# Kernel tuning notes

Hardware: AMD Instinct MI355X
Metric: run time of the kernel (lower is better)

The kernel has to match this reference:

```python
import jax, jax.numpy as jnp
import numpy as np

NEG = -1e30

def setup_inputs() -> dict:
    key = jax.random.key(0)
    ks = jax.random.split(key, 6)
    B, H, Lc, Lq = 32, 256, 1024, 256
    C = jax.random.normal(ks[0], (B, H, Lc), dtype=jnp.float32)
    Q = jax.random.normal(ks[1], (B, H, Lq), dtype=jnp.float32)
    cmask = jnp.ones((B, Lc), dtype=jnp.int32)
    qmask = jnp.ones((B, Lq), dtype=jnp.int32)
    # xavier_uniform on [3H,1]: bound = sqrt(6/(3H+1))
    bound = float(np.sqrt(6.0 / (3 * H + 1)))
    w = jax.random.uniform(ks[2], (3 * H,), minval=-bound, maxval=bound, dtype=jnp.float32)
    # kaiming_normal (relu, fan_in=4H): std = sqrt(2/(4H))
    W_res = jax.random.normal(ks[3], (H, 4 * H), dtype=jnp.float32) * float(np.sqrt(2.0 / (4 * H)))
    b_res = jnp.zeros((H,), dtype=jnp.float32)
    return {"C": C, "Q": Q, "cmask": cmask, "qmask": qmask, "w": w, "W_res": W_res, "b_res": b_res}

def reference(C, Q, cmask, qmask, w, W_res, b_res):
    H = w.shape[0] // 3
    Ct = jnp.transpose(C, (0, 2, 1))  # [B, Lc, H]
    Qt = jnp.transpose(Q, (0, 2, 1))  # [B, Lq, H]
    w1, w2, w3 = w[:H], w[H:2 * H], w[2 * H:]
    # trilinear similarity S[b,i,j] = Ct_i.w1 + Qt_j.w2 + (Ct_i*Qt_j).w3
    S = (jnp.einsum('blh,h->bl', Ct, w1)[:, :, None]
         + jnp.einsum('bmh,h->bm', Qt, w2)[:, None, :]
         + jnp.einsum('blh,bmh->blm', Ct * w3, Qt))  # [B, Lc, Lq]
    qm = qmask.astype(jnp.float32)[:, None, :]  # [B,1,Lq]
    cm = cmask.astype(jnp.float32)[:, :, None]  # [B,Lc,1]
    S_row = jax.nn.softmax(S + NEG * (1.0 - qm), axis=2)   # over questions
    S_col = jax.nn.softmax(S + NEG * (1.0 - cm), axis=1)   # over context
    A = jnp.einsum('blm,bmh->blh', S_row, Qt)  # [B, Lc, H]
    Bm = jnp.einsum('blm,bkm->blk', S_row, S_col)  # [B, Lc, Lc]
    Bv = jnp.einsum('blk,bkh->blh', Bm, Ct)  # [B, Lc, H]
    cat = jnp.concatenate([Ct, A, Ct * A, Ct * Bv], axis=2)  # [B, Lc, 4H]
    out = jax.nn.relu(jnp.einsum('blf,hf->blh', cat, W_res) + b_res)
    return jnp.transpose(out, (0, 2, 1))  # [B, H, Lc]
```

## Files before the change

### kernel.cpp

```cpp
#include <hip/hip_runtime.h>
#include <math.h>

#define NB 32
#define NH 256
#define NLC 1024
#define NLQ 256
#define NEGV (-1e30f)
#define TCH 8
#define KSPLIT 4

typedef short short8 __attribute__((ext_vector_type(8)));
typedef float f32x4 __attribute__((ext_vector_type(4)));

__device__ inline short bf16_of(float f) {
  union { float f; unsigned u; } v;
  v.f = f;
  unsigned r = (v.u + 0x7fffu + ((v.u >> 16) & 1u)) >> 16;
  return (short)r;
}
__device__ inline float f_of(short s) {
  union { unsigned u; float f; } v;
  v.u = ((unsigned)(unsigned short)s) << 16;
  return v.f;
}
__device__ inline short8 cvt8(float4 a, float4 b) {
  short8 o;
  o[0] = bf16_of(a.x); o[1] = bf16_of(a.y); o[2] = bf16_of(a.z); o[3] = bf16_of(a.w);
  o[4] = bf16_of(b.x); o[5] = bf16_of(b.y); o[6] = bf16_of(b.z); o[7] = bf16_of(b.w);
  return o;
}

#define XCD_SWZ(GX, GY, GZ, bx, by, bz)                                 \
  int bx, by, bz;                                                       \
  {                                                                     \
    int _lin = blockIdx.x + (GX) * (blockIdx.y + (GY) * blockIdx.z);    \
    const int _nwg = (GX) * (GY) * (GZ);                                \
    _lin = (_lin & 7) * (_nwg >> 3) + (_lin >> 3);                      \
    bx = _lin % (GX);                                                   \
    by = (_lin / (GX)) % (GY);                                          \
    bz = _lin / ((GX) * (GY));                                          \
  }

__device__ inline void lds_w8(short* lds, int r, int c, short8 v) {
  int byteoff = (r << 6) + (((c ^ ((r >> 1) & 3)) & 3) << 4);
  *(short8*)((char*)lds + byteoff) = v;
}
__device__ inline short8 lds_r8(const short* lds, int R, int g) {
  int byteoff = (R << 6) + (((g ^ ((R >> 1) & 3)) & 3) << 4);
  return *(const short8*)((const char*)lds + byteoff);
}
__device__ inline void stage_g(const short* src, int ld, short* lds, int t) {
  int L = t & 63, w = t >> 6;
  int cp = (L & 3) ^ ((L >> 3) & 3);
#pragma unroll
  for (int i = 0; i < 2; ++i) {
    int seg = w + i * 4;
    const short* g = src + (size_t)(seg * 16 + (L >> 2)) * ld + cp * 8;
    __builtin_amdgcn_global_load_lds(
        (const __attribute__((address_space(1))) unsigned int*)g,
        (__attribute__((address_space(3))) unsigned int*)(lds + seg * 512), 16,
        0, 0);
  }
}

#define GEMM_IDS                                       \
  int t = threadIdx.x, lane = t & 63, w = t >> 6;      \
  int ln = lane & 15, g = lane >> 4;                   \
  int wr = (w >> 1) << 6, wc = (w & 1) << 6;           \
  (void)wr; (void)wc;

#define MFMA_STEP(AS, BS)                                                      \
  {                                                                            \
    short8 af[4], bfr[4];                                                      \
    _Pragma("unroll") for (int mi = 0; mi < 4; ++mi) af[mi] =                  \
        lds_r8(AS, wr + mi * 16 + ln, g);                                      \
    _Pragma("unroll") for (int ni = 0; ni < 4; ++ni) bfr[ni] =                 \
        lds_r8(BS, wc + ni * 16 + ln, g);                                      \
    _Pragma("unroll") for (int mi = 0; mi < 4; ++mi)                           \
        _Pragma("unroll") for (int ni = 0; ni < 4; ++ni) acc[mi][ni] =         \
            __builtin_amdgcn_mfma_f32_16x16x32_bf16(af[mi], bfr[ni],           \
                                                    acc[mi][ni], 0, 0, 0);     \
  }

__global__ __launch_bounds__(256) void k_prep_c(const float* __restrict__ C,
                                                const float* __restrict__ w,
                                                short* __restrict__ Ct_lh,
                                                short* __restrict__ Cb_hl,
                                                float* __restrict__ s1p) {
  __shared__ float Ts[64][65];
  __shared__ float red[4][64];
  int b = blockIdx.z, h0 = blockIdx.y << 6, l0 = blockIdx.x << 6;
  int t = threadIdx.x;
  int hr = t >> 4, lc = (t & 15) << 2;
  const float* Cb = C + ((size_t)b * NH + h0) * NLC + l0;
#pragma unroll
  for (int i = 0; i < 4; ++i) {
    int h = hr + i * 16;
    float4 v = *(const float4*)&Cb[(size_t)h * NLC + lc];
    short4 cb;
    cb.x = bf16_of(v.x); cb.y = bf16_of(v.y);
    cb.z = bf16_of(v.z); cb.w = bf16_of(v.w);
    *(short4*)&Cb_hl[((size_t)b * NH + h0 + h) * NLC + l0 + lc] = cb;
    Ts[h][lc + 0] = v.x;
    Ts[h][lc + 1] = v.y;
    Ts[h][lc + 2] = v.z;
    Ts[h][lc + 3] = v.w;
  }
  __syncthreads();
  int lr = t >> 2, hc = (t & 3) << 4;
  short* dst = &Ct_lh[((size_t)b * NLC + l0 + lr) * NH + h0 + hc];
  short8 o0, o1;
#pragma unroll
  for (int j = 0; j < 8; ++j) o0[j] = bf16_of(Ts[hc + j][lr]);
#pragma unroll
  for (int j = 0; j < 8; ++j) o1[j] = bf16_of(Ts[hc + 8 + j][lr]);
  *(short8*)dst = o0;
  *(short8*)(dst + 8) = o1;
  int q = t >> 6, lq = t & 63;
  float a = 0.f;
#pragma unroll
  for (int j = 0; j < 16; ++j) a += Ts[(q << 4) + j][lq] * w[h0 + (q << 4) + j];
  red[q][lq] = a;
  __syncthreads();
  if (q == 0)
    s1p[((size_t)blockIdx.y * NB + b) * NLC + l0 + lq] =
        red[0][lq] + red[1][lq] + red[2][lq] + red[3][lq];
}

__global__ __launch_bounds__(256) void k_prep_q(const float* __restrict__ Q,
                                                const float* __restrict__ w,
                                                short* __restrict__ Qtw3,
                                                short* __restrict__ Qb_hm,
                                                float* __restrict__ s2p) {
  __shared__ float Ts[64][65];
  __shared__ float red[4][64];
  int b = blockIdx.z, h0 = blockIdx.y << 6, m0 = blockIdx.x << 6;
  int t = threadIdx.x;
  int hr = t >> 4, mc = (t & 15) << 2;
  const float* w3 = w + 2 * NH;
  const float* Qb = Q + ((size_t)b * NH + h0) * NLQ + m0;
#pragma unroll
  for (int i = 0; i < 4; ++i) {
    int h = hr + i * 16;
    float4 v = *(const float4*)&Qb[(size_t)h * NLQ + mc];
    short4 qb;
    qb.x = bf16_of(v.x); qb.y = bf16_of(v.y);
    qb.z = bf16_of(v.z); qb.w = bf16_of(v.w);
    *(short4*)&Qb_hm[((size_t)b * NH + h0 + h) * NLQ + m0 + mc] = qb;
    Ts[h][mc + 0] = v.x;
    Ts[h][mc + 1] = v.y;
    Ts[h][mc + 2] = v.z;
    Ts[h][mc + 3] = v.w;
  }
  __syncthreads();
  int mr = t >> 2, hc = (t & 3) << 4;
  short* dst = &Qtw3[((size_t)b * NLQ + m0 + mr) * NH + h0 + hc];
  short8 o0, o1;
#pragma unroll
  for (int j = 0; j < 8; ++j)
    o0[j] = bf16_of(Ts[hc + j][mr] * w3[h0 + hc + j]);
#pragma unroll
  for (int j = 0; j < 8; ++j)
    o1[j] = bf16_of(Ts[hc + 8 + j][mr] * w3[h0 + hc + 8 + j]);
  *(short8*)dst = o0;
  *(short8*)(dst + 8) = o1;
  int q = t >> 6, mq = t & 63;
  const float* w2 = w + NH;
  float a = 0.f;
#pragma unroll
  for (int j = 0; j < 16; ++j)
    a += Ts[(q << 4) + j][mq] * w2[h0 + (q << 4) + j];
  red[q][mq] = a;
  __syncthreads();
  if (q == 0)
    s2p[((size_t)blockIdx.y * NB + b) * NLQ + m0 + mq] =
        red[0][mq] + red[1][mq] + red[2][mq] + red[3][mq];
}

__global__ __launch_bounds__(256) void k_prep_bf16(const float* __restrict__ X,
                                                   short* __restrict__ Y) {
  size_t i = ((size_t)blockIdx.x * 256 + threadIdx.x) * 8;
  float4 v0 = *(const float4*)&X[i];
  float4 v1 = *(const float4*)&X[i + 4];
  *(short8*)&Y[i] = cvt8(v0, v1);
}

__global__ __launch_bounds__(256) void k_sgemm(
    const short* __restrict__ Ct_lh, const short* __restrict__ Qtw3,
    const float* __restrict__ s1p, const float* __restrict__ s2p,
    const int* __restrict__ cmask, float* __restrict__ S,
    float* __restrict__ pmax, float* __restrict__ psum) {
  __shared__ short As[2][4096], Bs[2][4096];
  __shared__ float cmsh[128];
  __shared__ float sredm[4][4][16], sreds[4][4][16];
  XCD_SWZ(NLQ / 128, NLC / 128, NB, bx, by, bz)
  int b = bz, l0 = by << 7, m0 = bx << 7;
  GEMM_IDS
  const short* Ag = Ct_lh + ((size_t)b * NLC + l0) * NH;
  const short* Bg = Qtw3 + ((size_t)b * NLQ + m0) * NH;
  f32x4 acc[4][4] = {};
  stage_g(Ag, NH, As[0], t);
  stage_g(Bg, NH, Bs[0], t);
  __syncthreads();
  int cur = 0;
  for (int kn = 32; kn <= NH; kn += 32) {
    if (kn < NH) {
      stage_g(Ag + kn, NH, As[cur ^ 1], t);
      stage_g(Bg + kn, NH, Bs[cur ^ 1], t);
    }
    MFMA_STEP(As[cur], Bs[cur])
    __syncthreads();
    cur ^= 1;
  }
  if (t < 128) cmsh[t] = cmask[b * NLC + l0 + t] ? 0.f : NEGV;
  __syncthreads();
  const int N1 = NB * NLC, N2 = NB * NLQ;
  float s1r[16], ncr[16];
#pragma unroll
  for (int mi = 0; mi < 4; ++mi)
#pragma unroll
    for (int r = 0; r < 4; ++r) {
      int lloc = wr + mi * 16 + g * 4 + r;
      int gl = b * NLC + l0 + lloc;
      s1r[mi * 4 + r] =
          s1p[gl] + s1p[N1 + gl] + s1p[2 * N1 + gl] + s1p[3 * N1 + gl];
      ncr[mi * 4 + r] = cmsh[lloc];
    }
  float s2v[4], mxc[4], smc[4];
#pragma unroll
  for (int ni = 0; ni < 4; ++ni) {
    int gm = b * NLQ + m0 + wc + ni * 16 + ln;
    s2v[ni] = s2p[gm] + s2p[N2 + gm] + s2p[2 * N2 + gm] + s2p[3 * N2 + gm];
    mxc[ni] = -INFINITY;
    smc[ni] = 0.f;
  }
#pragma unroll
  for (int ni = 0; ni < 4; ++ni)
#pragma unroll
    for (int mi = 0; mi < 4; ++mi)
#pragma unroll
      for (int r = 0; r < 4; ++r)
        mxc[ni] = fmaxf(mxc[ni],
                        acc[mi][ni][r] + s1r[mi * 4 + r] + s2v[ni] +
                            ncr[mi * 4 + r]);
#pragma unroll
  for (int ni = 0; ni < 4; ++ni) {
    int m = m0 + wc + ni * 16 + ln;
#pragma unroll
    for (int mi = 0; mi < 4; ++mi)
#pragma unroll
      for (int r = 0; r < 4; ++r) {
        int l = l0 + wr + mi * 16 + g * 4 + r;
        float sv = acc[mi][ni][r] + s1r[mi * 4 + r] + s2v[ni];
        S[((size_t)b * NLC + l) * NLQ + m] = sv;
        smc[ni] += expf(sv + ncr[mi * 4 + r] - mxc[ni]);
      }
  }
#pragma unroll
  for (int off = 16; off <= 32; off <<= 1)
#pragma unroll
    for (int ni = 0; ni < 4; ++ni) {
      float m2 = __shfl_xor(mxc[ni], off);
      float s2x = __shfl_xor(smc[ni], off);
      float nm = fmaxf(mxc[ni], m2);
      smc[ni] = smc[ni] * expf(mxc[ni] - nm) + s2x * expf(m2 - nm);
      mxc[ni] = nm;
    }
  if (lane < 16) {
#pragma unroll
    for (int ni = 0; ni < 4; ++ni) {
      sredm[w][ni][lane] = mxc[ni];
      sreds[w][ni][lane] = smc[ni];
    }
  }
  __syncthreads();
  if (t < 128) {
    int wcsel = t >> 6, nii = (t >> 4) & 3, lnn = t & 15;
    float mA = sredm[wcsel][nii][lnn], sA = sreds[wcsel][nii][lnn];
    float mB = sredm[wcsel + 2][nii][lnn], sB = sreds[wcsel + 2][nii][lnn];
    float nm = fmaxf(mA, mB);
    float sm = sA * expf(mA - nm) + sB * expf(mB - nm);
    int m = m0 + (wcsel << 6) + nii * 16 + lnn;
    size_t base = ((size_t)b * NLQ + m) * TCH + by;
    pmax[base] = nm;
    psum[base] = sm;
  }
}

__global__ __launch_bounds__(256) void k_colfin(const float* __restrict__ pmax,
                                                const float* __restrict__ psum,
                                                float* __restrict__ cmax,
                                                float* __restrict__ cinv) {
  int m = blockIdx.x * 256 + threadIdx.x;
  const float* pm = pmax + (size_t)m * TCH;
  const float* ps = psum + (size_t)m * TCH;
  float mx = pm[0], sm = ps[0];
#pragma unroll
  for (int c = 1; c < TCH; ++c) {
    float m2 = pm[c], s2 = ps[c];
    float nm = fmaxf(mx, m2);
    sm = sm * expf(mx - nm) + s2 * expf(m2 - nm);
    mx = nm;
  }
  cmax[m] = mx;
  cinv[m] = 1.0f / sm;
}

__global__ __launch_bounds__(256) void k_rowsoft(float* __restrict__ S,
                                                 const int* __restrict__ qmask,
                                                 const int* __restrict__ cmask,
                                                 const float* __restrict__ cmax,
                                                 const float* __restrict__ cinv) {
  int wave = threadIdx.x >> 6, lane = threadIdx.x & 63;
  int idx = (blockIdx.x << 2) + wave;
  int b = idx >> 10;
  float* row = S + (size_t)idx * NLQ;
  const int* qm = qmask + b * NLQ;
  int m4 = lane << 2;
  float4 v = *(const float4*)&row[m4];
  int4 q = *(const int4*)&qm[m4];
  float x0 = v.x + (q.x ? 0.f : NEGV);
  float x1 = v.y + (q.y ? 0.f : NEGV);
  float x2 = v.z + (q.z ? 0.f : NEGV);
  float x3 = v.w + (q.w ? 0.f : NEGV);
  float mx = fmaxf(fmaxf(x0, x1), fmaxf(x2, x3));
#pragma unroll
  for (int off = 32; off > 0; off >>= 1) mx = fmaxf(mx, __shfl_xor(mx, off));
  float p0 = expf(x0 - mx), p1 = expf(x1 - mx);
  float p2 = expf(x2 - mx), p3 = expf(x3 - mx);
  float sm = p0 + p1 + p2 + p3;
#pragma unroll
  for (int off = 32; off > 0; off >>= 1) sm += __shfl_xor(sm, off);
  float iv = 1.0f / sm;
  short4 o;
  o.x = bf16_of(p0 * iv);
  o.y = bf16_of(p1 * iv);
  o.z = bf16_of(p2 * iv);
  o.w = bf16_of(p3 * iv);
  float cmf = (float)cmask[idx];
  float4 cm4 = *(const float4*)&cmax[(b << 8) + m4];
  float4 ci4 = *(const float4*)&cinv[(b << 8) + m4];
  short4 oc;
  oc.x = bf16_of(expf(v.x - cm4.x) * ci4.x * cmf);
  oc.y = bf16_of(expf(v.y - cm4.y) * ci4.y * cmf);
  oc.z = bf16_of(expf(v.z - cm4.z) * ci4.z * cmf);
  oc.w = bf16_of(expf(v.w - cm4.w) * ci4.w * cmf);
  *(short4*)((short*)row + m4) = o;
  *(short4*)((short*)row + 256 + m4) = oc;
}

__global__ __launch_bounds__(256) void k_tgemm(const short* __restrict__ Cb_hl,
                                               const short* __restrict__ PcolS,
                                               short* __restrict__ Tpb) {
  __shared__ short As[4096], Bs[4096];
  XCD_SWZ(4, KSPLIT, NB, bx, by, bz)
  int b = bz;
  int ks = by;
  int h0 = (bx & 1) << 7;
  int m0 = (bx >> 1) << 7;
  GEMM_IDS
  const short* Ag = Cb_hl + ((size_t)b * NH + h0) * NLC;
  const short* Pb = PcolS + (size_t)b * NLC * 512 + 256 + m0;
  f32x4 acc[4][4] = {};
  int kbeg = ks * (NLC / KSPLIT), kend = kbeg + NLC / KSPLIT;
  int lloc = t >> 3, g2 = lloc >> 3, kin = lloc & 7;
  int mbase = (t & 7) << 4;
  for (int k0 = kbeg; k0 < kend; k0 += 32) {
    __syncthreads();
    stage_g(Ag + k0, NLC, As, t);
    {
      const short* srow = Pb + (size_t)(k0 + lloc) * 512;
      short8 x0 = *(const short8*)&srow[mbase];
      short8 x1 = *(const short8*)&srow[mbase + 8];
#pragma unroll
      for (int j = 0; j < 8; ++j) {
        int R = mbase + j;
        int byteoff =
            (R << 6) + (((g2 ^ ((R >> 1) & 3)) & 3) << 4) + (kin << 1);
        *(short*)((char*)Bs + byteoff) = x0[j];
      }
#pragma unroll
      for (int j = 0; j < 8; ++j) {
        int R = mbase + 8 + j;
        int byteoff =
            (R << 6) + (((g2 ^ ((R >> 1) & 3)) & 3) << 4) + (kin << 1);
        *(short*)((char*)Bs + byteoff) = x1[j];
      }
    }
    __syncthreads();
    MFMA_STEP(As, Bs)
  }
  short* dst = Tpb + ((size_t)ks * NB + b) * NH * NLQ;
#pragma unroll
  for (int mi = 0; mi < 4; ++mi)
#pragma unroll
    for (int ni = 0; ni < 4; ++ni)
#pragma unroll
      for (int r = 0; r < 4; ++r) {
        int h = h0 + wr + mi * 16 + g * 4 + r;
        int m = m0 + wc + ni * 16 + ln;
        dst[(size_t)h * NLQ + m] = bf16_of(acc[mi][ni][r]);
      }
}

__global__ __launch_bounds__(256) void k_tfin(const short* __restrict__ Tpb,
                                              short* __restrict__ Tt) {
  size_t i = ((size_t)blockIdx.x * 256 + threadIdx.x) * 8;
  const size_t stride = (size_t)NB * NH * NLQ;
  short8 x0 = *(const short8*)&Tpb[i];
  short8 x1 = *(const short8*)&Tpb[i + stride];
  short8 x2 = *(const short8*)&Tpb[i + 2 * stride];
  short8 x3 = *(const short8*)&Tpb[i + 3 * stride];
  short8 o;
#pragma unroll
  for (int j = 0; j < 8; ++j)
    o[j] = bf16_of(f_of(x0[j]) + f_of(x1[j]) + f_of(x2[j]) + f_of(x3[j]));
  *(short8*)&Tt[i] = o;
}

__global__ __launch_bounds__(256) void k_abgemm(
    const short* __restrict__ Prow, const short* __restrict__ Qb_hm,
    const short* __restrict__ Tt, const short* __restrict__ Ct_lh,
    short* __restrict__ A_lh, short* __restrict__ CtA_lh,
    short* __restrict__ CtBv_lh) {
  __shared__ short As[2][4096], Bs[2][4096];
  XCD_SWZ(4, NLC / 128, NB, bx, by, bz)
  int b = bz, l0 = by << 7, nb = bx;
  GEMM_IDS
  const short* Ag = Prow + ((size_t)b * NLC + l0) * 512;
  const short* Bbase = (nb < 2)
                           ? Qb_hm + ((size_t)b * NH + nb * 128) * NLQ
                           : Tt + ((size_t)b * NH + (nb - 2) * 128) * NLQ;
  f32x4 acc[4][4] = {};
  stage_g(Ag, 512, As[0], t);
  stage_g(Bbase, NLQ, Bs[0], t);
  __syncthreads();
  int cur = 0;
  for (int kn = 32; kn <= NLQ; kn += 32) {
    if (kn < NLQ) {
      stage_g(Ag + kn, 512, As[cur ^ 1], t);
      stage_g(Bbase + kn, NLQ, Bs[cur ^ 1], t);
    }
    MFMA_STEP(As[cur], Bs[cur])
    __syncthreads();
    cur ^= 1;
  }
  int hbase = (nb & 1) << 7;
  if (nb < 2) {
#pragma unroll
    for (int mi = 0; mi < 4; ++mi)
#pragma unroll
      for (int ni = 0; ni < 4; ++ni)
#pragma unroll
        for (int r = 0; r < 4; ++r) {
          int l = l0 + wr + mi * 16 + g * 4 + r;
          int h = hbase + wc + ni * 16 + ln;
          size_t off = ((size_t)b * NLC + l) * NH + h;
          float a = acc[mi][ni][r];
          A_lh[off] = bf16_of(a);
          CtA_lh[off] = bf16_of(f_of(Ct_lh[off]) * a);
        }
  } else {
#pragma unroll
    for (int mi = 0; mi < 4; ++mi)
#pragma unroll
      for (int ni = 0; ni < 4; ++ni)
#pragma unroll
        for (int r = 0; r < 4; ++r) {
          int l = l0 + wr + mi * 16 + g * 4 + r;
          int h = hbase + wc + ni * 16 + ln;
          size_t off = ((size_t)b * NLC + l) * NH + h;
          CtBv_lh[off] = bf16_of(f_of(Ct_lh[off]) * acc[mi][ni][r]);
        }
  }
}

__global__ __launch_bounds__(256) void k_out(
    const short* __restrict__ Wb, const short* __restrict__ Ct_lh,
    const short* __restrict__ A_lh, const short* __restrict__ CtA_lh,
    const short* __restrict__ CtBv_lh, const float* __restrict__ br,
    float* __restrict__ out) {
  __shared__ short As[2][4096], Bs[2][4096];
  XCD_SWZ(NLC / 128, NH / 128, NB, bx, by, bz)
  int b = bz, h0 = by << 7, l0 = bx << 7;
  GEMM_IDS
  const short* Wg = Wb + (size_t)h0 * (4 * NH);
  size_t boff = ((size_t)b * NLC + l0) * NH;
  f32x4 acc[4][4] = {};
  stage_g(Wg, 4 * NH, As[0], t);
  stage_g(Ct_lh + boff, NH, Bs[0], t);
  __syncthreads();
  int cur = 0;
  for (int kn = 32; kn <= 4 * NH; kn += 32) {
    bool has = kn < 4 * NH;
    if (has) {
      stage_g(Wg + kn, 4 * NH, As[cur ^ 1], t);
      int regn = kn >> 8, kon = kn & 255;
      const short* base = (regn == 0) ? Ct_lh
                          : (regn == 1) ? A_lh
                          : (regn == 2) ? CtA_lh : CtBv_lh;
      stage_g(base + boff + kon, NH, Bs[cur ^ 1], t);
    }
    MFMA_STEP(As[cur], Bs[cur])
    __syncthreads();
    cur ^= 1;
  }
#pragma unroll
  for (int mi = 0; mi < 4; ++mi)
#pragma unroll
    for (int ni = 0; ni < 4; ++ni) {
      int h = h0 + wr + mi * 16 + g * 4;
      int l = l0 + wc + ni * 16 + ln;
#pragma unroll
      for (int r = 0; r < 4; ++r) {
        float bias = br[h + r];
        out[((size_t)b * NH + h + r) * NLC + l] =
            fmaxf(acc[mi][ni][r] + bias, 0.f);
      }
    }
}

extern "C" void kernel_launch(void* const* d_in, const int* in_sizes, int n_in,
                              void* d_out, int out_size, void* d_ws,
                              size_t ws_size, hipStream_t stream) {
  (void)in_sizes;
  (void)n_in;
  (void)out_size;
  (void)ws_size;
  const float* C = (const float*)d_in[0];
  const float* Q = (const float*)d_in[1];
  const int* cmask = (const int*)d_in[2];
  const int* qmask = (const int*)d_in[3];
  const float* w = (const float*)d_in[4];
  const float* W = (const float*)d_in[5];
  const float* br = (const float*)d_in[6];
  float* out = (float*)d_out;

  char* p = (char*)d_ws;
  float* S = (float*)p;       p += (size_t)NB * NLC * NLQ * 4;
  short* Ct_lh = (short*)p;   p += (size_t)NB * NLC * NH * 2;
  short* A_lh = (short*)p;    p += (size_t)NB * NLC * NH * 2;
  short* CtBv_lh = (short*)p; p += (size_t)NB * NLC * NH * 2;
  short* CtA_lh = (short*)p;  p += (size_t)NB * NLC * NH * 2;
  short* Cb_hl = (short*)p;   p += (size_t)NB * NH * NLC * 2;
  short* Tt = (short*)p;      p += (size_t)NB * NH * NLQ * 2;
  short* Qtw3 = (short*)p;    p += (size_t)NB * NLQ * NH * 2;
  short* Qb_hm = (short*)p;   p += (size_t)NB * NH * NLQ * 2;
  short* Wb = (short*)p;      p += (size_t)NH * 4 * NH * 2;
  float* cmax = (float*)p;    p += (size_t)NB * NLQ * 4;
  float* cinv = (float*)p;    p += (size_t)NB * NLQ * 4;
  float* pmax = (float*)p;    p += (size_t)NB * NLQ * TCH * 4;
  float* psum = (float*)p;    p += (size_t)NB * NLQ * TCH * 4;
  float* s1p = (float*)p;     p += (size_t)4 * NB * NLC * 4;
  float* s2p = (float*)p;     p += (size_t)4 * NB * NLQ * 4;
  short* Tpb = A_lh;
  short* Prow = (short*)S;

  k_prep_c<<<dim3(NLC / 64, NH / 64, NB), dim3(256), 0, stream>>>(C, w, Ct_lh,
                                                                  Cb_hl, s1p);
  k_prep_q<<<dim3(NLQ / 64, NH / 64, NB), dim3(256), 0, stream>>>(
      Q, w, Qtw3, Qb_hm, s2p);
  k_prep_bf16<<<dim3(NH * 4 * NH / 2048), dim3(256), 0, stream>>>(W, Wb);
  k_sgemm<<<dim3(NLQ / 128, NLC / 128, NB), dim3(256), 0, stream>>>(
      Ct_lh, Qtw3, s1p, s2p, cmask, S, pmax, psum);
  k_colfin<<<dim3(NB * NLQ / 256), dim3(256), 0, stream>>>(pmax, psum, cmax,
                                                           cinv);
  k_rowsoft<<<dim3(NB * NLC / 4), dim3(256), 0, stream>>>(S, qmask, cmask,
                                                          cmax, cinv);
  k_tgemm<<<dim3(4, KSPLIT, NB), dim3(256), 0, stream>>>(Cb_hl, Prow, Tpb);
  k_tfin<<<dim3(NB * NH * NLQ / 2048), dim3(256), 0, stream>>>(Tpb, Tt);
  k_abgemm<<<dim3(4, NLC / 128, NB), dim3(256), 0, stream>>>(
      Prow, Qb_hm, Tt, Ct_lh, A_lh, CtA_lh, CtBv_lh);
  k_out<<<dim3(NLC / 128, NH / 128, NB), dim3(256), 0, stream>>>(
      Wb, Ct_lh, A_lh, CtA_lh, CtBv_lh, br, out);
}
```

Baseline: 136.1 us.

## Write transposed column-softmax via LDS and double-buffer tgemm staging

```diff
diff --git a/kernel.cpp b/kernel.cpp
--- a/kernel.cpp
+++ b/kernel.cpp
@@ -129,13 +129,25 @@
 
 __global__ __launch_bounds__(256) void k_prep_q(const float* __restrict__ Q,
                                                 const float* __restrict__ w,
+                                                const float* __restrict__ Wf,
                                                 short* __restrict__ Qtw3,
                                                 short* __restrict__ Qb_hm,
+                                                short* __restrict__ Wb,
                                                 float* __restrict__ s2p) {
   __shared__ float Ts[64][65];
   __shared__ float red[4][64];
   int b = blockIdx.z, h0 = blockIdx.y << 6, m0 = blockIdx.x << 6;
   int t = threadIdx.x;
+  {
+    size_t wi =
+        ((size_t)((blockIdx.z * 4 + blockIdx.y) * 4 + blockIdx.x) * 256 + t) *
+        2;
+    float2 wv = *(const float2*)&Wf[wi];
+    short2 ws2;
+    ws2.x = bf16_of(wv.x);
+    ws2.y = bf16_of(wv.y);
+    *(short2*)&Wb[wi] = ws2;
+  }
   int hr = t >> 4, mc = (t & 15) << 2;
   const float* w3 = w + 2 * NH;
   const float* Qb = Q + ((size_t)b * NH + h0) * NLQ + m0;
@@ -175,14 +187,6 @@
   if (q == 0)
     s2p[((size_t)blockIdx.y * NB + b) * NLQ + m0 + mq] =
         red[0][mq] + red[1][mq] + red[2][mq] + red[3][mq];
-}
-
-__global__ __launch_bounds__(256) void k_prep_bf16(const float* __restrict__ X,
-                                                   short* __restrict__ Y) {
-  size_t i = ((size_t)blockIdx.x * 256 + threadIdx.x) * 8;
-  float4 v0 = *(const float4*)&X[i];
-  float4 v1 = *(const float4*)&X[i + 4];
-  *(short8*)&Y[i] = cvt8(v0, v1);
 }
 
 __global__ __launch_bounds__(256) void k_sgemm(
@@ -306,53 +310,62 @@
   cinv[m] = 1.0f / sm;
 }
 
-__global__ __launch_bounds__(256) void k_rowsoft(float* __restrict__ S,
-                                                 const int* __restrict__ qmask,
-                                                 const int* __restrict__ cmask,
-                                                 const float* __restrict__ cmax,
-                                                 const float* __restrict__ cinv) {
-  int wave = threadIdx.x >> 6, lane = threadIdx.x & 63;
-  int idx = (blockIdx.x << 2) + wave;
-  int b = idx >> 10;
-  float* row = S + (size_t)idx * NLQ;
+__global__ __launch_bounds__(256) void k_colsoft(
+    float* __restrict__ S, const int* __restrict__ qmask,
+    const int* __restrict__ cmask, const float* __restrict__ cmax,
+    const float* __restrict__ cinv, short* __restrict__ PcolT) {
+  __shared__ short PT[64][258];
+  int b = blockIdx.z, l0 = blockIdx.x << 6;
+  int t = threadIdx.x, lane = t & 63, wv = t >> 6;
+  int m4 = lane << 2;
   const int* qm = qmask + b * NLQ;
-  int m4 = lane << 2;
-  float4 v = *(const float4*)&row[m4];
   int4 q = *(const int4*)&qm[m4];
-  float x0 = v.x + (q.x ? 0.f : NEGV);
-  float x1 = v.y + (q.y ? 0.f : NEGV);
-  float x2 = v.z + (q.z ? 0.f : NEGV);
-  float x3 = v.w + (q.w ? 0.f : NEGV);
-  float mx = fmaxf(fmaxf(x0, x1), fmaxf(x2, x3));
-#pragma unroll
-  for (int off = 32; off > 0; off >>= 1) mx = fmaxf(mx, __shfl_xor(mx, off));
-  float p0 = expf(x0 - mx), p1 = expf(x1 - mx);
-  float p2 = expf(x2 - mx), p3 = expf(x3 - mx);
-  float sm = p0 + p1 + p2 + p3;
-#pragma unroll
-  for (int off = 32; off > 0; off >>= 1) sm += __shfl_xor(sm, off);
-  float iv = 1.0f / sm;
-  short4 o;
-  o.x = bf16_of(p0 * iv);
-  o.y = bf16_of(p1 * iv);
-  o.z = bf16_of(p2 * iv);
-  o.w = bf16_of(p3 * iv);
-  float cmf = (float)cmask[idx];
+  float nq0 = q.x ? 0.f : NEGV, nq1 = q.y ? 0.f : NEGV;
+  float nq2 = q.z ? 0.f : NEGV, nq3 = q.w ? 0.f : NEGV;
   float4 cm4 = *(const float4*)&cmax[(b << 8) + m4];
   float4 ci4 = *(const float4*)&cinv[(b << 8) + m4];
-  short4 oc;
-  oc.x = bf16_of(expf(v.x - cm4.x) * ci4.x * cmf);
-  oc.y = bf16_of(expf(v.y - cm4.y) * ci4.y * cmf);
-  oc.z = bf16_of(expf(v.z - cm4.z) * ci4.z * cmf);
-  oc.w = bf16_of(expf(v.w - cm4.w) * ci4.w * cmf);
-  *(short4*)((short*)row + m4) = o;
-  *(short4*)((short*)row + 256 + m4) = oc;
+  for (int i = 0; i < 16; ++i) {
+    int lloc = wv * 16 + i;
+    int idx = b * NLC + l0 + lloc;
+    float* row = S + (size_t)idx * NLQ;
+    float4 v = *(const float4*)&row[m4];
+    float x0 = v.x + nq0, x1 = v.y + nq1, x2 = v.z + nq2, x3 = v.w + nq3;
+    float mx = fmaxf(fmaxf(x0, x1), fmaxf(x2, x3));
+#pragma unroll
+    for (int off = 32; off > 0; off >>= 1) mx = fmaxf(mx, __shfl_xor(mx, off));
+    float p0 = expf(x0 - mx), p1 = expf(x1 - mx);
+    float p2 = expf(x2 - mx), p3 = expf(x3 - mx);
+    float sm = p0 + p1 + p2 + p3;
+#pragma unroll
+    for (int off = 32; off > 0; off >>= 1) sm += __shfl_xor(sm, off);
+    float iv = 1.0f / sm;
+    short4 o;
+    o.x = bf16_of(p0 * iv);
+    o.y = bf16_of(p1 * iv);
+    o.z = bf16_of(p2 * iv);
+    o.w = bf16_of(p3 * iv);
+    *(short4*)((short*)row + m4) = o;
+    float cmf = cmask[idx] ? 1.f : 0.f;
+    PT[lloc][m4 + 0] = bf16_of(expf(v.x - cm4.x) * ci4.x * cmf);
+    PT[lloc][m4 + 1] = bf16_of(expf(v.y - cm4.y) * ci4.y * cmf);
+    PT[lloc][m4 + 2] = bf16_of(expf(v.z - cm4.z) * ci4.z * cmf);
+    PT[lloc][m4 + 3] = bf16_of(expf(v.w - cm4.w) * ci4.w * cmf);
+  }
+  __syncthreads();
+  short* dst = PcolT + ((size_t)b * NLQ + t) * NLC + l0;
+#pragma unroll
+  for (int j = 0; j < 8; ++j) {
+    short8 o8;
+#pragma unroll
+    for (int k = 0; k < 8; ++k) o8[k] = PT[j * 8 + k][t];
+    *(short8*)&dst[j * 8] = o8;
+  }
 }
 
 __global__ __launch_bounds__(256) void k_tgemm(const short* __restrict__ Cb_hl,
-                                               const short* __restrict__ PcolS,
+                                               const short* __restrict__ PcolT,
                                                short* __restrict__ Tpb) {
-  __shared__ short As[4096], Bs[4096];
+  __shared__ short As[2][4096], Bs[2][4096];
   XCD_SWZ(4, KSPLIT, NB, bx, by, bz)
   int b = bz;
   int ks = by;
@@ -360,35 +373,21 @@
   int m0 = (bx >> 1) << 7;
   GEMM_IDS
   const short* Ag = Cb_hl + ((size_t)b * NH + h0) * NLC;
-  const short* Pb = PcolS + (size_t)b * NLC * 512 + 256 + m0;
+  const short* Bg = PcolT + ((size_t)b * NLQ + m0) * NLC;
   f32x4 acc[4][4] = {};
   int kbeg = ks * (NLC / KSPLIT), kend = kbeg + NLC / KSPLIT;
-  int lloc = t >> 3, g2 = lloc >> 3, kin = lloc & 7;
-  int mbase = (t & 7) << 4;
-  for (int k0 = kbeg; k0 < kend; k0 += 32) {
+  stage_g(Ag + kbeg, NLC, As[0], t);
+  stage_g(Bg + kbeg, NLC, Bs[0], t);
+  __syncthreads();
+  int cur = 0;
+  for (int kn = kbeg + 32; kn <= kend; kn += 32) {
+    if (kn < kend) {
+      stage_g(Ag + kn, NLC, As[cur ^ 1], t);
+      stage_g(Bg + kn, NLC, Bs[cur ^ 1], t);
+    }
+    MFMA_STEP(As[cur], Bs[cur])
     __syncthreads();
-    stage_g(Ag + k0, NLC, As, t);
-    {
-      const short* srow = Pb + (size_t)(k0 + lloc) * 512;
-      short8 x0 = *(const short8*)&srow[mbase];
-      short8 x1 = *(const short8*)&srow[mbase + 8];
-#pragma unroll
-      for (int j = 0; j < 8; ++j) {
-        int R = mbase + j;
-        int byteoff =
-            (R << 6) + (((g2 ^ ((R >> 1) & 3)) & 3) << 4) + (kin << 1);
-        *(short*)((char*)Bs + byteoff) = x0[j];
-      }
-#pragma unroll
-      for (int j = 0; j < 8; ++j) {
-        int R = mbase + 8 + j;
-        int byteoff =
-            (R << 6) + (((g2 ^ ((R >> 1) & 3)) & 3) << 4) + (kin << 1);
-        *(short*)((char*)Bs + byteoff) = x1[j];
-      }
-    }
-    __syncthreads();
-    MFMA_STEP(As, Bs)
+    cur ^= 1;
   }
   short* dst = Tpb + ((size_t)ks * NB + b) * NH * NLQ;
 #pragma unroll
@@ -543,6 +542,7 @@
   short* CtBv_lh = (short*)p; p += (size_t)NB * NLC * NH * 2;
   short* CtA_lh = (short*)p;  p += (size_t)NB * NLC * NH * 2;
   short* Cb_hl = (short*)p;   p += (size_t)NB * NH * NLC * 2;
+  short* PcolT = (short*)p;   p += (size_t)NB * NLQ * NLC * 2;
   short* Tt = (short*)p;      p += (size_t)NB * NH * NLQ * 2;
   short* Qtw3 = (short*)p;    p += (size_t)NB * NLQ * NH * 2;
   short* Qb_hm = (short*)p;   p += (size_t)NB * NH * NLQ * 2;
@@ -559,15 +559,15 @@
   k_prep_c<<<dim3(NLC / 64, NH / 64, NB), dim3(256), 0, stream>>>(C, w, Ct_lh,
                                                                   Cb_hl, s1p);
   k_prep_q<<<dim3(NLQ / 64, NH / 64, NB), dim3(256), 0, stream>>>(
-      Q, w, Qtw3, Qb_hm, s2p);
-  k_prep_bf16<<<dim3(NH * 4 * NH / 2048), dim3(256), 0, stream>>>(W, Wb);
+      Q, w, W, Qtw3, Qb_hm, Wb, s2p);
   k_sgemm<<<dim3(NLQ / 128, NLC / 128, NB), dim3(256), 0, stream>>>(
       Ct_lh, Qtw3, s1p, s2p, cmask, S, pmax, psum);
   k_colfin<<<dim3(NB * NLQ / 256), dim3(256), 0, stream>>>(pmax, psum, cmax,
                                                            cinv);
-  k_rowsoft<<<dim3(NB * NLC / 4), dim3(256), 0, stream>>>(S, qmask, cmask,
-                                                          cmax, cinv);
-  k_tgemm<<<dim3(4, KSPLIT, NB), dim3(256), 0, stream>>>(Cb_hl, Prow, Tpb);
+  k_colsoft<<<dim3(NLC / 64, 1, NB), dim3(256), 0, stream>>>(S, qmask, cmask,
+                                                             cmax, cinv,
+                                                             PcolT);
+  k_tgemm<<<dim3(4, KSPLIT, NB), dim3(256), 0, stream>>>(Cb_hl, PcolT, Tpb);
   k_tfin<<<dim3(NB * NH * NLQ / 2048), dim3(256), 0, stream>>>(Tpb, Tt);
   k_abgemm<<<dim3(4, NLC / 128, NB), dim3(256), 0, stream>>>(
       Prow, Qb_hm, Tt, Ct_lh, A_lh, CtA_lh, CtBv_lh);
```

Measured after the change: 137.7 us. About the same (+1.2%).
